# Kernel optimization log

Measured on AMD Instinct MI355X. Metric: run time of the kernel, lower is better.

## Reference

```python
import jax, jax.numpy as jnp
import numpy as np
import math

STAGE_NUM = 5
EPS = 1e-6

def _l2norm(a, axis):
    return a / (EPS + jnp.linalg.norm(a, axis=axis, keepdims=True))

def setup_inputs() -> dict:
    key = jax.random.key(0)
    k1, k2, k3, k4 = jax.random.split(key, 4)
    b, n, c, h, w, k, out_c = 4, 4, 256, 64, 64, 128, 256
    x = jax.random.normal(k1, (b, c, h, w), dtype=jnp.float32)
    querys = jax.random.normal(k2, (b * n, c, h, w), dtype=jnp.float32)
    # mu init: normal(0, sqrt(2/k)) then l2norm over channel dim
    mu0 = jax.random.normal(k3, (1, c, k), dtype=jnp.float32) * math.sqrt(2.0 / k)
    mu0 = _l2norm(mu0, axis=1)
    # conv weight: normal(0, sqrt(2/(kh*kw*out_c)))
    fan = 3 * 3 * out_c
    conv_w = jax.random.normal(k4, (out_c, 2 * c, 3, 3), dtype=jnp.float32) * math.sqrt(2.0 / fan)
    conv_b = jnp.zeros((out_c,), dtype=jnp.float32)
    return {"x": x, "querys": querys, "mu0": mu0, "conv_w": conv_w, "conv_b": conv_b, "n": n}

def reference(x, querys, mu0, conv_w, conv_b, n):
    b, c, h, w = x.shape
    k = mu0.shape[2]
    xf = x.reshape(b, c, h * w)                       # [b, c, L]
    mu = jnp.broadcast_to(mu0, (b, c, k))

    # EM iterations (torch.no_grad -> stop_gradient)
    def em_step(mu, _):
        z = jnp.einsum('bcl,bck->blk', xf, mu)        # [b, L, k]
        z = jax.nn.softmax(z, axis=2)
        z_ = z / (EPS + jnp.sum(z, axis=1, keepdims=True))
        mu = jnp.einsum('bcl,blk->bck', xf, z_)       # [b, c, k]
        mu = _l2norm(mu, axis=1)
        return mu, None
    mu, _ = jax.lax.scan(em_step, mu, None, length=STAGE_NUM)
    mu = jax.lax.stop_gradient(mu)

    org_query = querys                                 # [b*n, c, h, w]
    q = querys.reshape(b, n, c, h, w).transpose(0, 2, 1, 3, 4).reshape(b, c, n * h * w)
    q_z = jax.nn.softmax(jnp.einsum('bcl,bck->blk', q, mu), axis=2)  # [b, nL, k]
    q_z = jax.lax.stop_gradient(q_z)

    rec = jnp.einsum('bck,blk->bcl', mu, q_z)          # [b, c, n*h*w]
    rec = rec.reshape(b, c, n, h, w).transpose(0, 2, 1, 3, 4).reshape(b * n, c, h, w)

    cat = jnp.concatenate((org_query, rec), axis=1)    # [b*n, 2c, h, w]
    out = jax.lax.conv_general_dilated(
        cat, conv_w, window_strides=(1, 1), padding='SAME',
        dimension_numbers=('NCHW', 'OIHW', 'NCHW'))
    out = out + conv_b[None, :, None, None]
    return (out, mu)
```

## Files before the change

### kernel.cpp

```cpp
#include <hip/hip_runtime.h>
#include <hip/hip_bf16.h>

#define B   4
#define NN  4
#define C   256
#define HH  64
#define WW  64
#define L   4096
#define NL  16384
#define K   128
#define OC  256
#define IC2 512
#define EPSV 1e-6f
#define PW  66
#define PA  4356

typedef __hip_bfloat16 bf16;
typedef __attribute__((ext_vector_type(8))) __bf16 bf16x8;
typedef __attribute__((ext_vector_type(4))) float f32x4;

#define AS1(p) ((const __attribute__((address_space(1))) void*)(p))
#define AS3(p) ((__attribute__((address_space(3))) void*)(p))

__global__ void k_init(const float* __restrict__ mu0, bf16* __restrict__ mub) {
    int i = blockIdx.x * 256 + threadIdx.x;
    int rem = i & 32767;
    int k = rem >> 8, c = rem & 255;
    mub[i] = __float2bfloat16(mu0[c * 128 + k]);
}

__global__ void k_prepx(const float* __restrict__ x, bf16* __restrict__ xb,
                        bf16* __restrict__ xt) {
    __shared__ float ld[64][65];
    int lt = blockIdx.x, ct = blockIdx.y, b = blockIdx.z;
    int t = threadIdx.x;
    #pragma unroll
    for (int i = 0; i < 16; i++) {
        int idx = t + i * 256;
        int ch = idx >> 6, xl = idx & 63;
        size_t a = ((size_t)b * C + ct * 64 + ch) * L + lt * 64 + xl;
        float v = x[a];
        ld[ch][xl] = v;
        xb[a] = __float2bfloat16(v);
    }
    __syncthreads();
    #pragma unroll
    for (int i = 0; i < 16; i++) {
        int idx = t + i * 256;
        int xl = idx >> 6, ch = idx & 63;
        xt[((size_t)b * L + lt * 64 + xl) * 256 + ct * 64 + ch] = __float2bfloat16(ld[ch][xl]);
    }
}

__global__ void k_mid(const float* __restrict__ qy, bf16* __restrict__ P2,
                      const float* __restrict__ cw, bf16* __restrict__ wb) {
    __shared__ float ld[64][65];
    int bid = blockIdx.x, t = threadIdx.x;
    if (bid < 4096) {
        int y = bid & 63, ct = (bid >> 6) & 3, img = bid >> 8;
        #pragma unroll
        for (int i = 0; i < 16; i++) {
            int idx = t + i * 256;
            int ch = idx >> 6, xl = idx & 63;
            ld[ch][xl] = qy[((size_t)img * C + ct * 64 + ch) * L + y * WW + xl];
        }
        __syncthreads();
        #pragma unroll
        for (int i = 0; i < 16; i++) {
            int idx = t + i * 256;
            int xl = idx >> 6, ch = idx & 63;
            P2[((size_t)img * PA + (size_t)(y + 1) * PW + xl + 1) * 512 + ct * 64 + ch] =
                __float2bfloat16(ld[ch][xl]);
        }
    } else if (bid < 5136) {
        int zi = bid - 4096;
        int img = zi / 65, grp = zi - img * 65;
        int pi = grp * 4 + (t >> 6), tt = t & 63;
        int y, x;
        if      (pi < 66)  { y = 0;        x = pi; }
        else if (pi < 132) { y = 65;       x = pi - 66; }
        else if (pi < 196) { y = pi - 131; x = 0; }
        else               { y = pi - 195; x = 65; }
        ((uint4*)P2)[((size_t)img * PA + (size_t)y * PW + x) * 64 + tt] = uint4{0, 0, 0, 0};
    } else {
        int idx = (bid - 5136) * 256 + t;
        int r  = idx / (OC * IC2);
        int oc = (idx / IC2) & 255;
        int ic = idx & 511;
        wb[idx] = __float2bfloat16(cw[((size_t)oc * IC2 + ic) * 9 + r]);
    }
}

__global__ void __launch_bounds__(256) k_z(const bf16* __restrict__ xt,
                                           const bf16* __restrict__ mub,
                                           bf16* __restrict__ zt) {
    __shared__ __align__(16) char smem[12288];
    char* tA = smem;
    char* tB = smem + 8192;
    int t = threadIdx.x, w = t >> 6, lane = t & 63;
    int b = blockIdx.y, l0 = blockIdx.x * 64;
    const bf16* Ab = mub + (size_t)b * K * C;
    const bf16* Bb = xt + ((size_t)b * L + l0) * C;
    int srow = t >> 2, sseg = t & 3, aseg = sseg ^ (srow & 3);
    char* dA0 = tA + w * 1024;
    char* dA1 = tA + 4096 + w * 1024;
    char* dB  = tB + w * 1024;
    int aoff[8], boff;
    #pragma unroll
    for (int i = 0; i < 8; i++) {
        int rowA = i * 16 + (lane & 15);
        aoff[i] = rowA * 64 + (((lane >> 4) ^ (rowA & 3)) << 4);
    }
    { int rowB = w * 16 + (lane & 15);
      boff = rowB * 64 + (((lane >> 4) ^ (rowB & 3)) << 4); }
    f32x4 acc[8];
    #pragma unroll
    for (int i = 0; i < 8; i++) acc[i] = f32x4{0.f, 0.f, 0.f, 0.f};
    for (int s = 0; s < 8; s++) {
        int cb0 = s * 32 + aseg * 8;
        __syncthreads();
        __builtin_amdgcn_global_load_lds(AS1(Ab + (size_t)srow * C + cb0),        AS3(dA0), 16, 0, 0);
        __builtin_amdgcn_global_load_lds(AS1(Ab + (size_t)(srow + 64) * C + cb0), AS3(dA1), 16, 0, 0);
        __builtin_amdgcn_global_load_lds(AS1(Bb + (size_t)srow * C + cb0),        AS3(dB),  16, 0, 0);
        __syncthreads();
        bf16x8 bfr = *(bf16x8*)(tB + boff);
        #pragma unroll
        for (int i = 0; i < 8; i++) {
            bf16x8 af = *(bf16x8*)(tA + aoff[i]);
            acc[i] = __builtin_amdgcn_mfma_f32_16x16x32_bf16(af, bfr, acc[i], 0, 0, 0);
        }
    }
    float m = -1e30f;
    #pragma unroll
    for (int i = 0; i < 8; i++)
        #pragma unroll
        for (int r = 0; r < 4; r++) m = fmaxf(m, acc[i][r]);
    m = fmaxf(m, __shfl_xor(m, 16, 64));
    m = fmaxf(m, __shfl_xor(m, 32, 64));
    float ssum = 0.f;
    #pragma unroll
    for (int i = 0; i < 8; i++)
        #pragma unroll
        for (int r = 0; r < 4; r++) { acc[i][r] = __expf(acc[i][r] - m); ssum += acc[i][r]; }
    ssum += __shfl_xor(ssum, 16, 64);
    ssum += __shfl_xor(ssum, 32, 64);
    float inv = 1.f / ssum;
    int quad = lane >> 4, col = lane & 15;
    bf16* zb = zt + (size_t)b * K * L + l0 + w * 16 + col;
    #pragma unroll
    for (int i = 0; i < 8; i++)
        #pragma unroll
        for (int r = 0; r < 4; r++) {
            int k = i * 16 + quad * 4 + r;
            zb[(size_t)k * L] = __float2bfloat16(acc[i][r] * inv);
        }
}

__global__ void __launch_bounds__(256) k_mu(const bf16* __restrict__ zt,
                                            const bf16* __restrict__ xb,
                                            float* __restrict__ part) {
    __shared__ __align__(16) char smem[12288];
    char* tA = smem;
    char* tB = smem + 8192;
    int t = threadIdx.x, w = t >> 6, lane = t & 63;
    int ct = blockIdx.x, chunk = blockIdx.y, b = blockIdx.z;
    const bf16* Ab = zt + (size_t)b * K * L + chunk * 256;
    const bf16* Bb = xb + ((size_t)b * C + ct * 64) * L + chunk * 256;
    int srow = t >> 2, sseg = t & 3, aseg = sseg ^ (srow & 3);
    char* dA0 = tA + w * 1024; char* dA1 = tA + 4096 + w * 1024;
    char* dB0 = tB + w * 1024;
    int wm = w >> 1, wn = w & 1;
    int aoff[4], boff[2];
    #pragma unroll
    for (int i = 0; i < 4; i++) {
        int rowA = wm * 64 + i * 16 + (lane & 15);
        aoff[i] = rowA * 64 + (((lane >> 4) ^ (rowA & 3)) << 4);
    }
    #pragma unroll
    for (int j = 0; j < 2; j++) {
        int rowB = wn * 32 + j * 16 + (lane & 15);
        boff[j] = rowB * 64 + (((lane >> 4) ^ (rowB & 3)) << 4);
    }
    f32x4 acc[4][2];
    #pragma unroll
    for (int i = 0; i < 4; i++)
        #pragma unroll
        for (int j = 0; j < 2; j++) acc[i][j] = f32x4{0.f, 0.f, 0.f, 0.f};
    for (int s = 0; s < 8; s++) {
        int lb = s * 32 + aseg * 8;
        __syncthreads();
        __builtin_amdgcn_global_load_lds(AS1(Ab + (size_t)srow * L + lb),        AS3(dA0), 16, 0, 0);
        __builtin_amdgcn_global_load_lds(AS1(Ab + (size_t)(srow + 64) * L + lb), AS3(dA1), 16, 0, 0);
        __builtin_amdgcn_global_load_lds(AS1(Bb + (size_t)srow * L + lb),        AS3(dB0), 16, 0, 0);
        __syncthreads();
        bf16x8 af[4], bfr[2];
        #pragma unroll
        for (int i = 0; i < 4; i++) af[i]  = *(bf16x8*)(tA + aoff[i]);
        #pragma unroll
        for (int j = 0; j < 2; j++) bfr[j] = *(bf16x8*)(tB + boff[j]);
        #pragma unroll
        for (int i = 0; i < 4; i++)
            #pragma unroll
            for (int j = 0; j < 2; j++)
                acc[i][j] = __builtin_amdgcn_mfma_f32_16x16x32_bf16(af[i], bfr[j], acc[i][j], 0, 0, 0);
    }
    float* pb = part + ((size_t)(b * 16 + chunk) * K) * C + ct * 64;
    int quad = lane >> 4, col = lane & 15;
    #pragma unroll
    for (int i = 0; i < 4; i++) {
        int k = wm * 64 + i * 16 + quad * 4;
        #pragma unroll
        for (int j = 0; j < 2; j++) {
            int c = wn * 32 + j * 16 + col;
            #pragma unroll
            for (int r = 0; r < 4; r++)
                pb[(size_t)(k + r) * C + c] = acc[i][j][r];
        }
    }
}

__global__ void k_norm(const float* __restrict__ part, bf16* __restrict__ mub,
                       bf16* __restrict__ muT, float* __restrict__ outT, int last) {
    int b = blockIdx.x >> 7, k = blockIdx.x & 127, lane = threadIdx.x;
    float v[4] = {0.f, 0.f, 0.f, 0.f};
    for (int ch = 0; ch < 16; ch++) {
        const float* p = part + ((size_t)(b * 16 + ch) * K + k) * C;
        #pragma unroll
        for (int j = 0; j < 4; j++) v[j] += p[lane + j * 64];
    }
    float s = v[0]*v[0] + v[1]*v[1] + v[2]*v[2] + v[3]*v[3];
    for (int o = 32; o > 0; o >>= 1) s += __shfl_xor(s, o, 64);
    float r = 1.f / (EPSV + sqrtf(s));
    bf16*  mb = mub + ((size_t)b * K + k) * C;
    bf16*  mt = muT + (size_t)b * C * K + k;
    #pragma unroll
    for (int j = 0; j < 4; j++) {
        float val = v[j] * r;
        int c = lane + j * 64;
        mb[c] = __float2bfloat16(val);
        mt[(size_t)c * K] = __float2bfloat16(val);
        if (last) outT[(size_t)b * 32768 + (size_t)c * 128 + k] = val;
    }
}

__global__ void __launch_bounds__(256) k_qzrec(const bf16* __restrict__ P2r,
                                               const bf16* __restrict__ mub,
                                               const bf16* __restrict__ muT,
                                               bf16* __restrict__ P2w) {
    __shared__ __align__(16) char smem[46080];
    char* tA = smem;
    char* tB = smem + 4096;
    char* zl = smem + 12288;
    char* mt = smem + 29696;
    int t = threadIdx.x, w = t >> 6, lane = t & 63;
    int b = blockIdx.y, tile = blockIdx.x;
    int n = tile >> 6, y = tile & 63;
    int img = b * NN + n;
    const bf16* Ab = P2r + ((size_t)img * PA + (size_t)(y + 1) * PW + 1) * 512;
    const bf16* Bb = mub + (size_t)b * K * C;
    int srow = t >> 2, sseg = t & 3, aseg = sseg ^ (srow & 3);
    char* dA  = tA + w * 1024;
    char* dB0 = tB + w * 1024;
    char* dB1 = tB + 4096 + w * 1024;
    int q = lane >> 4, col = lane & 15;
    int boff[8], aoff;
    #pragma unroll
    for (int j = 0; j < 8; j++) {
        int rowB = j * 16 + col;
        boff[j] = rowB * 64 + ((q ^ (rowB & 3)) << 4);
    }
    { int rowA = w * 16 + col;
      aoff = rowA * 64 + ((q ^ (rowA & 3)) << 4); }
    f32x4 acc[8];
    #pragma unroll
    for (int j = 0; j < 8; j++) acc[j] = f32x4{0.f, 0.f, 0.f, 0.f};
    for (int s = 0; s < 8; s++) {
        int cb0 = s * 32 + aseg * 8;
        __syncthreads();
        __builtin_amdgcn_global_load_lds(AS1(Ab + (size_t)srow * 512 + cb0),      AS3(dA),  16, 0, 0);
        __builtin_amdgcn_global_load_lds(AS1(Bb + (size_t)srow * C + cb0),        AS3(dB0), 16, 0, 0);
        __builtin_amdgcn_global_load_lds(AS1(Bb + (size_t)(srow + 64) * C + cb0), AS3(dB1), 16, 0, 0);
        __syncthreads();
        bf16x8 af = *(bf16x8*)(tA + aoff);
        #pragma unroll
        for (int j = 0; j < 8; j++) {
            bf16x8 bfr = *(bf16x8*)(tB + boff[j]);
            acc[j] = __builtin_amdgcn_mfma_f32_16x16x32_bf16(af, bfr, acc[j], 0, 0, 0);
        }
    }
    #pragma unroll
    for (int r = 0; r < 4; r++) {
        float mm = acc[0][r];
        #pragma unroll
        for (int j = 1; j < 8; j++) mm = fmaxf(mm, acc[j][r]);
        mm = fmaxf(mm, __shfl_xor(mm, 1, 64));
        mm = fmaxf(mm, __shfl_xor(mm, 2, 64));
        mm = fmaxf(mm, __shfl_xor(mm, 4, 64));
        mm = fmaxf(mm, __shfl_xor(mm, 8, 64));
        float ss = 0.f;
        float e[8];
        #pragma unroll
        for (int j = 0; j < 8; j++) { e[j] = __expf(acc[j][r] - mm); ss += e[j]; }
        ss += __shfl_xor(ss, 1, 64);
        ss += __shfl_xor(ss, 2, 64);
        ss += __shfl_xor(ss, 4, 64);
        ss += __shfl_xor(ss, 8, 64);
        float inv = 1.f / ss;
        int zrow = w * 16 + q * 4 + r;
        #pragma unroll
        for (int j = 0; j < 8; j++)
            *(bf16*)(zl + zrow * 272 + (j * 16 + col) * 2) = __float2bfloat16(e[j] * inv);
    }
    const bf16* Mb = muT + (size_t)b * C * K;
    auto stageMT = [&](int p) {
        int s = p >> 1, h = p & 1;
        #pragma unroll
        for (int it2 = 0; it2 < 2; it2++) {
            int u = it2 * 256 + t;
            int row = u >> 2, seg = u & 3;
            int grow = h * 128 + row;
            int sg = seg ^ ((grow ^ (grow >> 2)) & 3);
            __builtin_amdgcn_global_load_lds(AS1(Mb + (size_t)grow * K + s * 32 + sg * 8),
                AS3(mt + h * 8192 + it2 * 4096 + w * 1024), 16, 0, 0);
        }
    };
    stageMT(0);
    stageMT(1);
    bf16x8 afz[4];
    #pragma unroll
    for (int ch = 0; ch < 4; ch++)
        afz[ch] = *(bf16x8*)(zl + (w * 16 + col) * 272 + ch * 64 + q * 16);
    f32x4 acc2[16];
    #pragma unroll
    for (int j = 0; j < 16; j++) acc2[j] = f32x4{0.f, 0.f, 0.f, 0.f};
    #pragma unroll
    for (int p = 0; p < 8; p++) {
        if (p < 7) asm volatile("s_waitcnt vmcnt(2)" ::: "memory");
        else       asm volatile("s_waitcnt vmcnt(0)" ::: "memory");
        __builtin_amdgcn_s_barrier();
        asm volatile("" ::: "memory");
        const int s = p >> 1, h = p & 1;
        #pragma unroll
        for (int jj = 0; jj < 8; jj++) {
            int j = h * 8 + jj;
            int rr = j * 16 + col;
            int local = rr - h * 128;
            bf16x8 bm = *(bf16x8*)(mt + h * 8192 + local * 64 +
                                   ((q ^ ((rr ^ (rr >> 2)) & 3)) << 4));
            acc2[j] = __builtin_amdgcn_mfma_f32_16x16x32_bf16(afz[s], bm, acc2[j], 0, 0, 0);
        }
        asm volatile("" ::: "memory");
        __builtin_amdgcn_s_barrier();
        asm volatile("" ::: "memory");
        if (p < 6) stageMT(p + 2);
    }
    #pragma unroll
    for (int r = 0; r < 4; r++) {
        int xg = w * 16 + q * 4 + r;
        bf16* dst = P2w + ((size_t)img * PA + (size_t)(y + 1) * PW + xg + 1) * 512 + 256;
        #pragma unroll
        for (int j = 0; j < 16; j++)
            dst[j * 16 + col] = __float2bfloat16(acc2[j][r]);
    }
}

__global__ void __launch_bounds__(256, 2) k_conv(const bf16* __restrict__ P2,
                                                 const bf16* __restrict__ Wb,
                                                 const float* __restrict__ cb,
                                                 float* __restrict__ out) {
    __shared__ __align__(16) char smem[49920];
    char* inl = smem;
    char* wld = smem + 25344;
    int t = threadIdx.x, w = t >> 6, lane = t & 63;
    int m0  = blockIdx.x * 128;
    int y0  = blockIdx.y * 4;
    int img = blockIdx.z;
    int srow = t >> 2;
    int aseg = (t & 3) ^ ((srow ^ (srow >> 2)) & 3);
    int wm = w >> 1, wn = w & 1;
    int q = lane >> 4, lane15 = lane & 15;

    int aoff[4];
    #pragma unroll
    for (int i = 0; i < 4; i++) {
        int rowA = wm * 64 + i * 16 + lane15;
        aoff[i] = rowA * 64 + (((q ^ (rowA ^ (rowA >> 2))) & 3) << 4);
    }

    auto stageIN = [&](int cc) {
        size_t ibase = (size_t)img * PA * 512 + cc * 32;
        #pragma unroll
        for (int it = 0; it < 6; it++) {
            unsigned g = it * 256 + t;
            unsigned row = g / 264u, ps = g - row * 264u;
            unsigned px = ps >> 2, s0 = ps & 3;
            unsigned sg = s0 ^ ((px ^ (px >> 1)) & 3);
            __builtin_amdgcn_global_load_lds(
                AS1(P2 + ibase + ((size_t)(y0 + row) * PW + px) * 512 + sg * 8),
                AS3(inl + it * 4096 + w * 1024), 16, 0, 0);
        }
        if (t < 48) {
            unsigned g = 1536 + t;
            unsigned row = g / 264u, ps = g - row * 264u;
            unsigned px = ps >> 2, s0 = ps & 3;
            unsigned sg = s0 ^ ((px ^ (px >> 1)) & 3);
            __builtin_amdgcn_global_load_lds(
                AS1(P2 + ibase + ((size_t)(y0 + row) * PW + px) * 512 + sg * 8),
                AS3(inl + 24576), 16, 0, 0);
        }
    };

    f32x4 acc[4][8];
    #pragma unroll
    for (int i = 0; i < 4; i++) {
        int oc = m0 + wm * 64 + i * 16 + q * 4;
        #pragma unroll
        for (int r = 0; r < 4; r++) {
            float bv = cb[oc + r];
            #pragma unroll
            for (int j = 0; j < 8; j++) acc[i][j][r] = bv;
        }
    }

    stageIN(0);
    {
        const bf16* w0 = Wb + (size_t)(m0 + srow) * IC2 + aseg * 8;
        __builtin_amdgcn_global_load_lds(AS1(w0),                         AS3(wld + w * 1024), 16, 0, 0);
        __builtin_amdgcn_global_load_lds(AS1(w0 + (size_t)64 * IC2),      AS3(wld + 4096 + w * 1024), 16, 0, 0);
        const bf16* w1 = w0 + (size_t)(OC * IC2);
        __builtin_amdgcn_global_load_lds(AS1(w1),                         AS3(wld + 8192 + w * 1024), 16, 0, 0);
        __builtin_amdgcn_global_load_lds(AS1(w1 + (size_t)64 * IC2),      AS3(wld + 8192 + 4096 + w * 1024), 16, 0, 0);
    }
    asm volatile("s_waitcnt vmcnt(0)" ::: "memory");
    __builtin_amdgcn_s_barrier();
    asm volatile("" ::: "memory");

    for (int cc = 0; cc < 16; cc++) {
        #pragma unroll
        for (int rt = 0; rt < 9; rt++) {
            const int dy = rt / 3, dx = rt % 3;
            char* wbuf = wld + (rt % 3) * 8192;
            bf16x8 af[4];
            #pragma unroll
            for (int i = 0; i < 4; i++) af[i] = *(bf16x8*)(wbuf + aoff[i]);
            const bool doPf = (cc * 9 + rt + 2) < 144;
            if (doPf) {
                const int g2 = rt + 2;
                const int rt2 = (g2 >= 9) ? g2 - 9 : g2;
                const int cc2 = cc + (g2 >= 9 ? 1 : 0);
                char* wdst = wld + ((rt + 2) % 3) * 8192;
                const bf16* wsrc = Wb + (size_t)rt2 * (OC * IC2) + (size_t)(m0 + srow) * IC2
                                 + cc2 * 32 + aseg * 8;
                __builtin_amdgcn_global_load_lds(AS1(wsrc),                    AS3(wdst + w * 1024), 16, 0, 0);
                __builtin_amdgcn_global_load_lds(AS1(wsrc + (size_t)64 * IC2), AS3(wdst + 4096 + w * 1024), 16, 0, 0);
            }
            __builtin_amdgcn_s_setprio(1);
            #pragma unroll
            for (int j = 0; j < 8; j++) {
                int p = (j & 3) * 16 + lane15 + dx;
                int rowsel = 2 * wn + (j >> 2) + dy;
                bf16x8 bfr = *(bf16x8*)(inl + rowsel * 4224 + p * 64 +
                                        (((q ^ (p ^ (p >> 1))) & 3) << 4));
                #pragma unroll
                for (int i = 0; i < 4; i++)
                    acc[i][j] = __builtin_amdgcn_mfma_f32_16x16x32_bf16(af[i], bfr, acc[i][j], 0, 0, 0);
            }
            __builtin_amdgcn_s_setprio(0);
            if (rt == 8) {
                if (cc < 15) {
                    asm volatile("" ::: "memory");
                    __builtin_amdgcn_s_barrier();
                    asm volatile("" ::: "memory");
                    stageIN(cc + 1);
                    asm volatile("s_waitcnt vmcnt(0)" ::: "memory");
                    __builtin_amdgcn_s_barrier();
                    asm volatile("" ::: "memory");
                }
            } else {
                if (doPf) asm volatile("s_waitcnt vmcnt(2)" ::: "memory");
                else      asm volatile("s_waitcnt vmcnt(0)" ::: "memory");
                __builtin_amdgcn_s_barrier();
                asm volatile("" ::: "memory");
            }
        }
    }

    #pragma unroll
    for (int i = 0; i < 4; i++) {
        int oc = m0 + wm * 64 + i * 16 + q * 4;
        #pragma unroll
        for (int j = 0; j < 8; j++) {
            int px = blockIdx.y * 256 + wn * 128 + (j >> 2) * 64 + (j & 3) * 16 + lane15;
            #pragma unroll
            for (int r = 0; r < 4; r++)
                out[((size_t)img * OC + oc + r) * L + px] = acc[i][j][r];
        }
    }
}

extern "C" void kernel_launch(void* const* d_in, const int* in_sizes, int n_in,
                              void* d_out, int out_size, void* d_ws, size_t ws_size,
                              hipStream_t stream) {
    const float* x   = (const float*)d_in[0];
    const float* qy  = (const float*)d_in[1];
    const float* mu0 = (const float*)d_in[2];
    const float* cw  = (const float*)d_in[3];
    const float* cb  = (const float*)d_in[4];
    float* out = (float*)d_out;

    char* ws = (char*)d_ws;
    bf16*  mu_b = (bf16*) (ws + 524288);
    bf16*  muT  = (bf16*) (ws + 786432);
    bf16*  Wb   = (bf16*) (ws + 1048576);
    bf16*  zt   = (bf16*) (ws + 3407872);
    bf16*  P2   = (bf16*) (ws + 20185088);
    bf16*  x_bf = (bf16*) (ws + 20185088);
    float* part = (float*)(ws + 20185088 + 8388608);
    bf16*  xt   = (bf16*) (ws + 20185088 + 16777216);

    k_init<<<512, 256, 0, stream>>>(mu0, mu_b);
    k_prepx<<<dim3(64, 4, 4), 256, 0, stream>>>(x, x_bf, xt);

    for (int it = 0; it < 5; it++) {
        k_z<<<dim3(64, 4), 256, 0, stream>>>(xt, mu_b, zt);
        k_mu<<<dim3(4, 16, 4), 256, 0, stream>>>(zt, x_bf, part);
        k_norm<<<512, 64, 0, stream>>>(part, mu_b, muT, out + 16777216, it == 4 ? 1 : 0);
    }

    k_mid<<<9744, 256, 0, stream>>>(qy, P2, cw, Wb);

    k_qzrec<<<dim3(256, 4), 256, 0, stream>>>(P2, mu_b, muT, P2);
    k_conv<<<dim3(2, 16, 16), 256, 0, stream>>>(P2, Wb, cb, out);
}
```

Before: 393.9 us.

## Fuse EM iterations and prep stages into one cooperative persistent kernel

Replaces the init, prep, 5×(z, mu, norm) and mid-stage launches with a single cooperative kernel of 256 blocks that uses grid-wide syncs between phases. This removes about 17 kernel launches and their inter-kernel gaps. In exchange, each phase is capped at 256 blocks, so k_mid's 9744-block work now runs in a grid-stride loop with less parallelism, and every grid sync has its own cost. The old multi-launch path is kept as a fallback if the cooperative launch fails.

```diff
diff --git a/kernel.cpp b/kernel.cpp
--- a/kernel.cpp
+++ b/kernel.cpp
@@ -1,5 +1,6 @@
 #include <hip/hip_runtime.h>
 #include <hip/hip_bf16.h>
+#include <hip/hip_cooperative_groups.h>
 
 #define B   4
 #define NN  4
@@ -22,11 +23,233 @@
 #define AS1(p) ((const __attribute__((address_space(1))) void*)(p))
 #define AS3(p) ((__attribute__((address_space(3))) void*)(p))
 
+__global__ void __launch_bounds__(256) k_em(
+    const float* __restrict__ x, const float* __restrict__ qy,
+    const float* __restrict__ mu0, const float* __restrict__ cw,
+    bf16* __restrict__ mub, bf16* __restrict__ muT, bf16* __restrict__ Wb,
+    bf16* __restrict__ zt, bf16* __restrict__ P2,
+    bf16* __restrict__ x_bf, bf16* __restrict__ xt,
+    float* __restrict__ part, float* __restrict__ outT)
+{
+    cooperative_groups::grid_group gg = cooperative_groups::this_grid();
+    __shared__ __align__(16) char smem[16640];
+    char* tA = smem;
+    char* tB = smem + 8192;
+    float (*ld)[65] = (float(*)[65])smem;
+    int bid = blockIdx.x, t = threadIdx.x, w = t >> 6, lane = t & 63;
+    int srow = t >> 2, aseg = (t & 3) ^ (srow & 3);
+    int quad = lane >> 4, col = lane & 15;
+
+    for (int i = bid * 256 + t; i < 131072; i += 65536) {
+        int rem = i & 32767;
+        mub[i] = __float2bfloat16(mu0[(rem & 255) * 128 + (rem >> 8)]);
+    }
+    for (int v = bid; v < 1024; v += 256) {
+        int lt = v & 63, ct = (v >> 6) & 3, b = v >> 8;
+        #pragma unroll
+        for (int i = 0; i < 16; i++) {
+            int idx = t + i * 256;
+            int ch = idx >> 6, xl = idx & 63;
+            size_t a = ((size_t)b * C + ct * 64 + ch) * L + lt * 64 + xl;
+            float vv = x[a];
+            ld[ch][xl] = vv;
+            x_bf[a] = __float2bfloat16(vv);
+        }
+        __syncthreads();
+        #pragma unroll
+        for (int i = 0; i < 16; i++) {
+            int idx = t + i * 256;
+            int xl = idx >> 6, ch = idx & 63;
+            xt[((size_t)b * L + lt * 64 + xl) * 256 + ct * 64 + ch] = __float2bfloat16(ld[ch][xl]);
+        }
+        __syncthreads();
+    }
+    gg.sync();
+
+    const int zb_ = bid >> 6, zl0 = (bid & 63) << 6;
+    const bf16* zAb = mub + (size_t)zb_ * K * C;
+    const bf16* zBb = xt + ((size_t)zb_ * L + zl0) * C;
+    char* zdA0 = tA + w * 1024;
+    char* zdA1 = tA + 4096 + w * 1024;
+    char* zdB  = tB + w * 1024;
+    int zaoff[8], zboff;
+    #pragma unroll
+    for (int i = 0; i < 8; i++) {
+        int rowA = i * 16 + col;
+        zaoff[i] = rowA * 64 + ((quad ^ (rowA & 3)) << 4);
+    }
+    { int rowB = w * 16 + col;
+      zboff = rowB * 64 + ((quad ^ (rowB & 3)) << 4); }
+
+    const int mct = bid & 3, mchunk = (bid >> 2) & 15, mb_ = bid >> 6;
+    const bf16* mAb = zt + (size_t)mb_ * K * L + mchunk * 256;
+    const bf16* mBb = x_bf + ((size_t)mb_ * C + mct * 64) * L + mchunk * 256;
+    char* mdA0 = tA + w * 1024; char* mdA1 = tA + 4096 + w * 1024;
+    char* mdB0 = tB + w * 1024;
+    const int wm = w >> 1, wn = w & 1;
+    int maoff[4], mboff[2];
+    #pragma unroll
+    for (int i = 0; i < 4; i++) {
+        int rowA = wm * 64 + i * 16 + col;
+        maoff[i] = rowA * 64 + ((quad ^ (rowA & 3)) << 4);
+    }
+    #pragma unroll
+    for (int j = 0; j < 2; j++) {
+        int rowB = wn * 32 + j * 16 + col;
+        mboff[j] = rowB * 64 + ((quad ^ (rowB & 3)) << 4);
+    }
+
+    for (int it = 0; it < 5; it++) {
+        {
+            f32x4 acc[8];
+            #pragma unroll
+            for (int i = 0; i < 8; i++) acc[i] = f32x4{0.f, 0.f, 0.f, 0.f};
+            for (int s = 0; s < 8; s++) {
+                int cb0 = s * 32 + aseg * 8;
+                __syncthreads();
+                __builtin_amdgcn_global_load_lds(AS1(zAb + (size_t)srow * C + cb0),        AS3(zdA0), 16, 0, 0);
+                __builtin_amdgcn_global_load_lds(AS1(zAb + (size_t)(srow + 64) * C + cb0), AS3(zdA1), 16, 0, 0);
+                __builtin_amdgcn_global_load_lds(AS1(zBb + (size_t)srow * C + cb0),        AS3(zdB),  16, 0, 0);
+                __syncthreads();
+                bf16x8 bfr = *(bf16x8*)(tB + zboff);
+                #pragma unroll
+                for (int i = 0; i < 8; i++) {
+                    bf16x8 af = *(bf16x8*)(tA + zaoff[i]);
+                    acc[i] = __builtin_amdgcn_mfma_f32_16x16x32_bf16(af, bfr, acc[i], 0, 0, 0);
+                }
+            }
+            float m = -1e30f;
+            #pragma unroll
+            for (int i = 0; i < 8; i++)
+                #pragma unroll
+                for (int r = 0; r < 4; r++) m = fmaxf(m, acc[i][r]);
+            m = fmaxf(m, __shfl_xor(m, 16, 64));
+            m = fmaxf(m, __shfl_xor(m, 32, 64));
+            float ssum = 0.f;
+            #pragma unroll
+            for (int i = 0; i < 8; i++)
+                #pragma unroll
+                for (int r = 0; r < 4; r++) { acc[i][r] = __expf(acc[i][r] - m); ssum += acc[i][r]; }
+            ssum += __shfl_xor(ssum, 16, 64);
+            ssum += __shfl_xor(ssum, 32, 64);
+            float inv = 1.f / ssum;
+            bf16* zb = zt + (size_t)zb_ * K * L + zl0 + w * 16 + col;
+            #pragma unroll
+            for (int i = 0; i < 8; i++)
+                #pragma unroll
+                for (int r = 0; r < 4; r++) {
+                    int k = i * 16 + quad * 4 + r;
+                    zb[(size_t)k * L] = __float2bfloat16(acc[i][r] * inv);
+                }
+        }
+        gg.sync();
+        {
+            f32x4 acc[4][2];
+            #pragma unroll
+            for (int i = 0; i < 4; i++)
+                #pragma unroll
+                for (int j = 0; j < 2; j++) acc[i][j] = f32x4{0.f, 0.f, 0.f, 0.f};
+            for (int s = 0; s < 8; s++) {
+                int lb = s * 32 + aseg * 8;
+                __syncthreads();
+                __builtin_amdgcn_global_load_lds(AS1(mAb + (size_t)srow * L + lb),        AS3(mdA0), 16, 0, 0);
+                __builtin_amdgcn_global_load_lds(AS1(mAb + (size_t)(srow + 64) * L + lb), AS3(mdA1), 16, 0, 0);
+                __builtin_amdgcn_global_load_lds(AS1(mBb + (size_t)srow * L + lb),        AS3(mdB0), 16, 0, 0);
+                __syncthreads();
+                bf16x8 af[4], bfr[2];
+                #pragma unroll
+                for (int i = 0; i < 4; i++) af[i]  = *(bf16x8*)(tA + maoff[i]);
+                #pragma unroll
+                for (int j = 0; j < 2; j++) bfr[j] = *(bf16x8*)(tB + mboff[j]);
+                #pragma unroll
+                for (int i = 0; i < 4; i++)
+                    #pragma unroll
+                    for (int j = 0; j < 2; j++)
+                        acc[i][j] = __builtin_amdgcn_mfma_f32_16x16x32_bf16(af[i], bfr[j], acc[i][j], 0, 0, 0);
+            }
+            float* pb = part + ((size_t)(mb_ * 16 + mchunk) * K) * C + mct * 64;
+            #pragma unroll
+            for (int i = 0; i < 4; i++) {
+                int k = wm * 64 + i * 16 + quad * 4;
+                #pragma unroll
+                for (int j = 0; j < 2; j++) {
+                    int c = wn * 32 + j * 16 + col;
+                    #pragma unroll
+                    for (int r = 0; r < 4; r++)
+                        pb[(size_t)(k + r) * C + c] = acc[i][j][r];
+                }
+            }
+        }
+        gg.sync();
+        if (w < 2) {
+            int pair = bid * 2 + w;
+            int b = pair >> 7, k = pair & 127;
+            float v0 = 0.f, v1 = 0.f, v2 = 0.f, v3 = 0.f;
+            #pragma unroll
+            for (int ch = 0; ch < 16; ch++) {
+                const float* p = part + ((size_t)(b * 16 + ch) * K + k) * C;
+                v0 += p[lane]; v1 += p[lane + 64]; v2 += p[lane + 128]; v3 += p[lane + 192];
+            }
+            float s = v0*v0 + v1*v1 + v2*v2 + v3*v3;
+            for (int o = 32; o > 0; o >>= 1) s += __shfl_xor(s, o, 64);
+            float r = 1.f / (EPSV + sqrtf(s));
+            bf16* mb = mub + ((size_t)b * K + k) * C;
+            bf16* mt = muT + (size_t)b * C * K + k;
+            float vv[4] = {v0, v1, v2, v3};
+            #pragma unroll
+            for (int j = 0; j < 4; j++) {
+                float val = vv[j] * r;
+                int c = lane + j * 64;
+                mb[c] = __float2bfloat16(val);
+                mt[(size_t)c * K] = __float2bfloat16(val);
+                if (it == 4) outT[(size_t)b * 32768 + (size_t)c * 128 + k] = val;
+            }
+        }
+        gg.sync();
+    }
+
+    for (int v = bid; v < 9744; v += 256) {
+        if (v < 4096) {
+            int y = v & 63, ct = (v >> 6) & 3, img = v >> 8;
+            #pragma unroll
+            for (int i = 0; i < 16; i++) {
+                int idx = t + i * 256;
+                int ch = idx >> 6, xl = idx & 63;
+                ld[ch][xl] = qy[((size_t)img * C + ct * 64 + ch) * L + y * WW + xl];
+            }
+            __syncthreads();
+            #pragma unroll
+            for (int i = 0; i < 16; i++) {
+                int idx = t + i * 256;
+                int xl = idx >> 6, ch = idx & 63;
+                P2[((size_t)img * PA + (size_t)(y + 1) * PW + xl + 1) * 512 + ct * 64 + ch] =
+                    __float2bfloat16(ld[ch][xl]);
+            }
+            __syncthreads();
+        } else if (v < 5136) {
+            int zi = v - 4096;
+            int img = zi / 65, grp = zi - img * 65;
+            int pi = grp * 4 + (t >> 6), tt = t & 63;
+            int y, xx;
+            if      (pi < 66)  { y = 0;        xx = pi; }
+            else if (pi < 132) { y = 65;       xx = pi - 66; }
+            else if (pi < 196) { y = pi - 131; xx = 0; }
+            else               { y = pi - 195; xx = 65; }
+            ((uint4*)P2)[((size_t)img * PA + (size_t)y * PW + xx) * 64 + tt] = uint4{0, 0, 0, 0};
+        } else {
+            int idx = (v - 5136) * 256 + t;
+            int r  = idx / (OC * IC2);
+            int oc = (idx / IC2) & 255;
+            int ic = idx & 511;
+            Wb[idx] = __float2bfloat16(cw[((size_t)oc * IC2 + ic) * 9 + r]);
+        }
+    }
+}
+
 __global__ void k_init(const float* __restrict__ mu0, bf16* __restrict__ mub) {
     int i = blockIdx.x * 256 + threadIdx.x;
     int rem = i & 32767;
-    int k = rem >> 8, c = rem & 255;
-    mub[i] = __float2bfloat16(mu0[c * 128 + k]);
+    mub[i] = __float2bfloat16(mu0[(rem & 255) * 128 + (rem >> 8)]);
 }
 
 __global__ void k_prepx(const float* __restrict__ x, bf16* __restrict__ xb,
@@ -223,6 +446,7 @@
                        bf16* __restrict__ muT, float* __restrict__ outT, int last) {
     int b = blockIdx.x >> 7, k = blockIdx.x & 127, lane = threadIdx.x;
     float v[4] = {0.f, 0.f, 0.f, 0.f};
+    #pragma unroll
     for (int ch = 0; ch < 16; ch++) {
         const float* p = part + ((size_t)(b * 16 + ch) * K + k) * C;
         #pragma unroll
@@ -517,17 +741,23 @@
     bf16*  x_bf = (bf16*) (ws + 20185088);
     float* part = (float*)(ws + 20185088 + 8388608);
     bf16*  xt   = (bf16*) (ws + 20185088 + 16777216);
-
-    k_init<<<512, 256, 0, stream>>>(mu0, mu_b);
-    k_prepx<<<dim3(64, 4, 4), 256, 0, stream>>>(x, x_bf, xt);
-
-    for (int it = 0; it < 5; it++) {
-        k_z<<<dim3(64, 4), 256, 0, stream>>>(xt, mu_b, zt);
-        k_mu<<<dim3(4, 16, 4), 256, 0, stream>>>(zt, x_bf, part);
-        k_norm<<<512, 64, 0, stream>>>(part, mu_b, muT, out + 16777216, it == 4 ? 1 : 0);
-    }
-
-    k_mid<<<9744, 256, 0, stream>>>(qy, P2, cw, Wb);
+    float* outT = out + 16777216;
+
+    void* args[] = {(void*)&x, (void*)&qy, (void*)&mu0, (void*)&cw,
+                    (void*)&mu_b, (void*)&muT, (void*)&Wb, (void*)&zt, (void*)&P2,
+                    (void*)&x_bf, (void*)&xt, (void*)&part, (void*)&outT};
+    hipError_t ce = hipLaunchCooperativeKernel((const void*)k_em, dim3(256), dim3(256),
+                                               args, 0, stream);
+    if (ce != hipSuccess) {
+        k_init<<<512, 256, 0, stream>>>(mu0, mu_b);
+        k_prepx<<<dim3(64, 4, 4), 256, 0, stream>>>(x, x_bf, xt);
+        for (int it = 0; it < 5; it++) {
+            k_z<<<dim3(64, 4), 256, 0, stream>>>(xt, mu_b, zt);
+            k_mu<<<dim3(4, 16, 4), 256, 0, stream>>>(zt, x_bf, part);
+            k_norm<<<512, 64, 0, stream>>>(part, mu_b, muT, outT, it == 4 ? 1 : 0);
+        }
+        k_mid<<<9744, 256, 0, stream>>>(qy, P2, cw, Wb);
+    }
 
     k_qzrec<<<dim3(256, 4), 256, 0, stream>>>(P2, mu_b, muT, P2);
     k_conv<<<dim3(2, 16, 16), 256, 0, stream>>>(P2, Wb, cb, out);
```

After: 992.6 us. +152.0%, slower.
